# Kernel tuning notes

Measured on AMD Instinct MI355X. Metric: run time of the kernel, lower is better.

## Reference

```python
import jax, jax.numpy as jnp
import numpy as np

BIG_NEG = -1e9


def setup_inputs() -> dict:
    key = jax.random.key(0)
    ks = jax.random.split(key, 6)
    b, N1, d, C1, K = 4, 511, 64, 31, 32
    features = jax.random.normal(ks[0], (b, N1, d), jnp.float32)
    transition_logits = jax.random.normal(ks[1], (C1, C1), jnp.float32)
    init_logits = jax.random.uniform(ks[2], (C1,), jnp.float32)
    poisson_log_rates = jax.random.normal(ks[3], (C1,), jnp.float32) * 0.5 + 1.5
    A = jax.random.normal(ks[5], (d, d), jnp.float32)
    gaussian_cov = jnp.eye(d, dtype=jnp.float32) + 0.1 * (A @ A.T) / d
    gaussian_means = jax.random.normal(ks[4], (C1, d), jnp.float32) * 0.1
    return {
        "features": features,
        "transition_logits": transition_logits,
        "init_logits": init_logits,
        "poisson_log_rates": poisson_log_rates,
        "gaussian_means": gaussian_means,
        "gaussian_cov": gaussian_cov,
        "max_k": K,
        "add_eos": 1,
    }


def reference(features, transition_logits, init_logits, poisson_log_rates,
              gaussian_means, gaussian_cov, max_k, add_eos):
    b, N1, d = features.shape
    C1 = transition_logits.shape[0]
    K = int(max_k)
    dt = features.dtype

    # transition log-probs: mask diagonal with BIG_NEG, normalize over axis 0 (torch dim=0)
    trans = jax.nn.log_softmax(
        jnp.where(jnp.eye(C1, dtype=bool), jnp.asarray(BIG_NEG, dt), transition_logits), axis=0)
    init = jax.nn.log_softmax(init_logits)

    # Poisson duration log-probs: k*log(rate) - rate - lgamma(k+1), k = 0..K-1
    rates = jnp.exp(poisson_log_rates)  # [C1]
    tsteps = jnp.arange(K, dtype=dt)[:, None]  # [K,1]
    length = tsteps * poisson_log_rates[None, :] - rates[None, :] - jax.scipy.special.gammaln(tsteps + 1.0)  # [K,C1]

    # Gaussian emission log-probs, shared full covariance across classes
    L = jnp.linalg.cholesky(gaussian_cov)
    Linv = jax.scipy.linalg.solve_triangular(L, jnp.eye(d, dtype=dt), lower=True)
    diff = features[:, :, None, :] - gaussian_means[None, None]          # [b,N1,C1,d]
    y = jnp.einsum('bncd,ed->bnce', diff, Linv)
    maha = jnp.sum(y * y, axis=-1)                                       # [b,N1,C1]
    logdet = 2.0 * jnp.sum(jnp.log(jnp.diag(L)))
    emis = -0.5 * (d * jnp.log(jnp.asarray(2.0 * jnp.pi, dt)) + logdet + maha)

    if add_eos:
        N, C = N1 + 1, C1 + 1
        trans_a = jnp.full((C, C), BIG_NEG, dt).at[:C1, :C1].set(trans).at[C1, :].set(0.0)
        init_a = jnp.full((C,), BIG_NEG, dt).at[:C1].set(init)
        length_a = jnp.full((K, C), BIG_NEG, dt).at[:, :C1].set(length).at[1, C1].set(0.0)
        emis_a = jnp.full((b, N, C), BIG_NEG, dt).at[:, :N1, :C1].set(emis).at[:, N1, C1].set(0.0)
    else:
        N, C = N1, C1
        trans_a, init_a, length_a, emis_a = trans, init, length, emis

    ep = jnp.pad(emis_a, ((0, 0), (0, K), (0, 0)))
    cs = jnp.concatenate([jnp.zeros((b, 1, C), dt), jnp.cumsum(ep, axis=1)], axis=1)  # [b,N+K+1,C]
    tt = jnp.arange(N - 1)[:, None]
    kk = jnp.arange(K)[None, :]
    win = cs[:, tt + kk] - cs[:, tt]  # [b, N-1, K, C]

    # edge scores: b x (N-1) x K x C_prev x C
    scores = (trans_a[None, None, None] +
              length_a[None, None, :, None, :] +
              win[:, :, :, None, :])
    scores = scores.at[:, 0].add(init_a[None, None, None, :])
    keos = jnp.arange(1, K)
    scores = scores.at[:, N - 1 - keos, keos].add(emis_a[:, N - 1][:, None, :, None])
    return scores
```

## Files before the change

### kernel.cpp

```cpp
#include <hip/hip_runtime.h>
#include <math.h>

#define BIG_NEG -1.0e9f

typedef float f4 __attribute__((ext_vector_type(4)));

constexpr int B  = 4;
constexpr int N1 = 511;
constexpr int C1 = 31;
constexpr int K  = 32;
constexpr int N  = N1 + 1;
constexpr int C  = C1 + 1;

constexpr int WS_TRANS = 0;
constexpr int WS_INIT  = 1024;
constexpr int WS_LEN   = 1056;
constexpr int WS_P     = 2080;
constexpr int WS_W     = 6176;
constexpr int WS_BIAS  = 8224;
constexpr int WS_EMIS  = 8256;

__global__ __launch_bounds__(512) void k_prep(const float* __restrict__ tl,
                                              const float* __restrict__ il,
                                              const float* __restrict__ plr,
                                              const float* __restrict__ cov,
                                              const float* __restrict__ means,
                                              float* __restrict__ ws) {
    __shared__ float M[64][132];
    __shared__ float fc[2][64];
    __shared__ float piv[64];
    __shared__ float rpiv_s[64];
    __shared__ float mu[C1][64];
    __shared__ float s_logdet;

    const int tid = threadIdx.x;
    const int ii = tid >> 3;
    const int cg = tid & 7;

    f4* Mrow = (f4*)&M[ii][0];

    for (int idx = tid; idx < 1024; idx += 512) {
        const int i = idx >> 5, j = idx & 31;
        float lv;
        if (j < C1) {
            float lr = plr[j];
            lv = (float)i * lr - expf(lr) - lgammaf((float)i + 1.0f);
        } else {
            lv = (i == 1) ? 0.0f : BIG_NEG;
        }
        ws[WS_LEN + idx] = lv;
        if (i == C1) ws[WS_TRANS + idx] = 0.0f;
        else if (j == C1) ws[WS_TRANS + idx] = BIG_NEG;
    }
    if (tid < B * C) {
        const int bb = tid >> 5, cc = tid & 31;
        ws[WS_EMIS + (bb * N + N1) * C + cc] = (cc == C1) ? 0.0f : BIG_NEG;
    }
    if (tid < C1) {
        const int jj = tid;
        float m = BIG_NEG;
        for (int r = 0; r < C1; ++r) {
            float v = (r == jj) ? BIG_NEG : tl[r * C1 + jj];
            m = fmaxf(m, v);
        }
        float s = 0.0f;
        for (int r = 0; r < C1; ++r) {
            float v = (r == jj) ? BIG_NEG : tl[r * C1 + jj];
            s += expf(v - m);
        }
        float lse = m + logf(s);
        for (int r = 0; r < C1; ++r) {
            float v = (r == jj) ? BIG_NEG : tl[r * C1 + jj];
            ws[WS_TRANS + r * 32 + jj] = v - lse;
        }
    }
    if (tid == 32) {
        float m = -1.0e30f;
        for (int cc = 0; cc < C1; ++cc) m = fmaxf(m, il[cc]);
        float s = 0.0f;
        for (int cc = 0; cc < C1; ++cc) s += expf(il[cc] - m);
        float lse = m + logf(s);
        for (int cc = 0; cc < C1; ++cc) ws[WS_INIT + cc] = il[cc] - lse;
        ws[WS_INIT + C1] = BIG_NEG;
    }

    {
        Mrow[cg]     = *(const f4*)&cov[ii * 64 + 4 * cg];
        Mrow[cg + 8] = *(const f4*)&cov[ii * 64 + 4 * (cg + 8)];
        const int r0 = 4 * cg, r1 = 4 * (cg + 8);
        f4 e1 = {(ii == r0) ? 1.f : 0.f, (ii == r0 + 1) ? 1.f : 0.f,
                 (ii == r0 + 2) ? 1.f : 0.f, (ii == r0 + 3) ? 1.f : 0.f};
        f4 e2 = {(ii == r1) ? 1.f : 0.f, (ii == r1 + 1) ? 1.f : 0.f,
                 (ii == r1 + 2) ? 1.f : 0.f, (ii == r1 + 3) ? 1.f : 0.f};
        Mrow[cg + 16] = e1;
        Mrow[cg + 24] = e2;
    }
    if (cg == 0) fc[0][ii] = cov[ii * 64];
    for (int idx = tid; idx < C1 * 64; idx += 512)
        mu[idx >> 6][idx & 63] = means[idx];
    __syncthreads();

    for (int jj = 0; jj < 64; ++jj) {
        const int par = jj & 1;
        const float p = fc[par][jj];
        const float f = fc[par][ii] / p;
        if (tid == 0) piv[jj] = p;
        const f4* Mjj = (const f4*)&M[jj][0];
        const bool upd = (ii != jj);
#pragma unroll
        for (int h = 0; h < 4; ++h) {
            const int q = cg + 8 * h;
            const int k0 = 4 * q;
            const bool active = (k0 < 64) ? (k0 + 3 >= jj) : (k0 - 64 <= jj);
            if (!active) continue;
            f4 v = Mrow[q];
            if (upd) {
                v = v - f * Mjj[q];
                Mrow[q] = v;
            }
            if (jj < 63 && (unsigned)(jj + 1 - k0) < 4u) {
                const int d = jj + 1 - k0;
                fc[par ^ 1][ii] = (d == 0) ? v.x : (d == 1) ? v.y
                                 : (d == 2) ? v.z : v.w;
            }
        }
        __syncthreads();
    }

    if (tid < 64) {
        float lp = logf(piv[tid]);
        rpiv_s[tid] = 1.0f / piv[tid];
        for (int m2 = 32; m2 >= 1; m2 >>= 1) lp += __shfl_xor(lp, m2, 64);
        if (tid == 0) s_logdet = lp;
    }
    __syncthreads();

    {
        const float rp = rpiv_s[ii];
        f4 a = Mrow[16 + cg] * rp;
        f4 b = Mrow[24 + cg] * rp;
        *(f4*)&ws[WS_P + ii * 64 + 4 * cg] = a;
        *(f4*)&ws[WS_P + ii * 64 + 32 + 4 * cg] = b;
    }

    {
        const int c = tid >> 4;
        const int l = tid & 15;
        if (c < C1) {
            const f4* muc = (const f4*)&mu[c][0];
            float qacc = 0.0f;
#pragma unroll
            for (int h = 0; h < 4; ++h) {
                const int dd = l + 16 * h;
                const f4* Mr = (const f4*)&M[dd][64];
                f4 a4 = {0.f, 0.f, 0.f, 0.f};
#pragma unroll
                for (int e4 = 0; e4 < 16; ++e4) a4 += Mr[e4] * muc[e4];
                float a = (a4.x + a4.y) + (a4.z + a4.w);
                a *= rpiv_s[dd];
                ws[WS_W + dd * 32 + c] = a;
                qacc += a * mu[c][dd];
            }
            for (int m2 = 8; m2 >= 1; m2 >>= 1) qacc += __shfl_xor(qacc, m2, 64);
            if (l == 0)
                ws[WS_BIAS + c] =
                    -0.5f * (64.0f * 1.8378770664093453f + s_logdet + qacc);
        }
    }
}

__global__ __launch_bounds__(256) void k_emis(const float* __restrict__ feat,
                                              float* __restrict__ ws) {
    const int tid = threadIdx.x;
    const int w = tid >> 6, lane = tid & 63;
    const int flat = blockIdx.x * 4 + w;
    const int b = flat / N1, n = flat % N1;
    __shared__ float xs[4][64];

    const float x = feat[flat * 64 + lane];
    xs[w][lane] = x;

    const float* __restrict__ P = ws + WS_P;
    float z = 0.0f;
    for (int dd = 0; dd < 64; ++dd) z += P[dd * 64 + lane] * xs[w][dd];

    float xz = x * z;
    for (int m = 32; m >= 1; m >>= 1) xz += __shfl_xor(xz, m);

    float val = BIG_NEG;
    if (lane < C1) {
        float s = ws[WS_BIAS + lane] - 0.5f * xz;
        const float* __restrict__ wT = ws + WS_W;
        for (int dd = 0; dd < 64; ++dd) s += wT[dd * 32 + lane] * xs[w][dd];
        val = s;
    }
    if (lane < C) ws[WS_EMIS + (b * N + n) * C + lane] = val;
}

__global__ __launch_bounds__(256) void k_main(const float* __restrict__ ws,
                                              float* __restrict__ out) {
    const int bid = blockIdx.x;
    const int b = bid / N1, t = bid % N1;
    const int tid = threadIdx.x;
    __shared__ float sh[32][36];

    {
        const int row = tid >> 3;
        const int c4 = (tid & 7) << 2;
        f4 v = {0.f, 0.f, 0.f, 0.f};
        if (t + row < N)
            v = *(const f4*)&ws[WS_EMIS + (b * N + t + row) * C + c4];
        *(f4*)&sh[row][c4] = v;
    }
    __syncthreads();

    {
        const int sc = tid >> 3;
        const int g  = tid & 7;
        float p0 = sh[4 * g + 0][sc];
        float p1 = p0 + sh[4 * g + 1][sc];
        float p2 = p1 + sh[4 * g + 2][sc];
        float p3 = p2 + sh[4 * g + 3][sc];
        float sum = p3;
#pragma unroll
        for (int off = 1; off < 8; off <<= 1) {
            float nv = __shfl_up(sum, off, 8);
            if (g >= off) sum += nv;
        }
        const float excl = sum - p3;
        sh[4 * g + 0][sc] = p0 + excl;
        sh[4 * g + 1][sc] = p1 + excl;
        sh[4 * g + 2][sc] = p2 + excl;
        sh[4 * g + 3][sc] = p3 + excl;
    }

    const int cp = tid >> 3;
    const int c0 = (tid & 7) << 2;
    f4 pre = *(const f4*)&ws[WS_TRANS + cp * 32 + c0];
    if (t == 0) {
        f4 in4 = *(const f4*)&ws[WS_INIT + c0];
        pre = pre + in4;
    }
    const float emisN = (cp == C1) ? 0.0f : BIG_NEG;
    const int keos = N1 - t;
    const size_t obase = (size_t)bid * (K * C * C) + (size_t)(cp * 32 + c0);
    __syncthreads();

#pragma unroll 4
    for (int k = 0; k < K; ++k) {
        f4 len4 = *(const f4*)&ws[WS_LEN + k * 32 + c0];
        f4 w4 = {0.f, 0.f, 0.f, 0.f};
        if (k > 0) w4 = *(const f4*)&sh[k - 1][c0];
        f4 o = pre + len4 + w4;
        if (k == keos) o = o + emisN;
        *(f4*)&out[obase + (size_t)k * (C * C)] = o;
    }
}

extern "C" void kernel_launch(void* const* d_in, const int* in_sizes, int n_in,
                              void* d_out, int out_size, void* d_ws, size_t ws_size,
                              hipStream_t stream) {
    const float* feat = (const float*)d_in[0];
    const float* tl   = (const float*)d_in[1];
    const float* il   = (const float*)d_in[2];
    const float* plr  = (const float*)d_in[3];
    const float* gm   = (const float*)d_in[4];
    const float* gc   = (const float*)d_in[5];
    float* ws  = (float*)d_ws;
    float* out = (float*)d_out;

    hipLaunchKernelGGL(k_prep, dim3(1), dim3(512), 0, stream, tl, il, plr, gc, gm, ws);
    hipLaunchKernelGGL(k_emis, dim3(B * N1 / 4), dim3(256), 0, stream, feat, ws);
    hipLaunchKernelGGL(k_main, dim3(B * N1), dim3(256), 0, stream, ws, out);
}
```

Baseline: 98.66 us.

## Fuse emission computation into main kernel and block Cholesky elimination by two

Removes the separate emission kernel. Each main-kernel block now recomputes the emission log-probs for its 32-row window directly from the features, using P and a transposed W layout in the workspace. This saves a launch and the global round trip, at the cost of recomputing each emission row up to 32 times. The single-block Gauss-Jordan elimination in the prep kernel now processes two pivots per step with reciprocal intrinsics, halving the number of block barriers on that serial critical path.

Result: slower. 246.3 us (+149.6%).

```diff
diff --git a/kernel.cpp b/kernel.cpp
--- a/kernel.cpp
+++ b/kernel.cpp
@@ -16,9 +16,8 @@
 constexpr int WS_INIT  = 1024;
 constexpr int WS_LEN   = 1056;
 constexpr int WS_P     = 2080;
-constexpr int WS_W     = 6176;
+constexpr int WS_W2    = 6176;
 constexpr int WS_BIAS  = 8224;
-constexpr int WS_EMIS  = 8256;
 
 __global__ __launch_bounds__(512) void k_prep(const float* __restrict__ tl,
                                               const float* __restrict__ il,
@@ -27,7 +26,8 @@
                                               const float* __restrict__ means,
                                               float* __restrict__ ws) {
     __shared__ float M[64][132];
-    __shared__ float fc[2][64];
+    __shared__ float cA[2][64];
+    __shared__ float cB[2][64];
     __shared__ float piv[64];
     __shared__ float rpiv_s[64];
     __shared__ float mu[C1][64];
@@ -51,10 +51,6 @@
         ws[WS_LEN + idx] = lv;
         if (i == C1) ws[WS_TRANS + idx] = 0.0f;
         else if (j == C1) ws[WS_TRANS + idx] = BIG_NEG;
-    }
-    if (tid < B * C) {
-        const int bb = tid >> 5, cc = tid & 31;
-        ws[WS_EMIS + (bb * N + N1) * C + cc] = (cc == C1) ? 0.0f : BIG_NEG;
     }
     if (tid < C1) {
         const int jj = tid;
@@ -95,33 +91,53 @@
         Mrow[cg + 16] = e1;
         Mrow[cg + 24] = e2;
     }
-    if (cg == 0) fc[0][ii] = cov[ii * 64];
+    if (cg == 0) {
+        cA[0][ii] = cov[ii * 64];
+        cB[0][ii] = cov[ii * 64 + 1];
+    }
     for (int idx = tid; idx < C1 * 64; idx += 512)
         mu[idx >> 6][idx & 63] = means[idx];
     __syncthreads();
 
-    for (int jj = 0; jj < 64; ++jj) {
-        const int par = jj & 1;
-        const float p = fc[par][jj];
-        const float f = fc[par][ii] / p;
-        if (tid == 0) piv[jj] = p;
-        const f4* Mjj = (const f4*)&M[jj][0];
-        const bool upd = (ii != jj);
+    for (int s = 0; s < 64; s += 2) {
+        const int par = (s >> 1) & 1;
+        const float a1   = cA[par][ii];
+        const float b1   = cB[par][ii];
+        const float p1   = cA[par][s];
+        const float cb_s = cB[par][s];
+        const float a1p  = cA[par][s + 1];
+        const float b1p  = cB[par][s + 1];
+        const float rp1 = __builtin_amdgcn_rcpf(p1);
+        const float f1_i = a1 * rp1;
+        const float f1_p = a1p * rp1;
+        const float p2 = b1p - f1_p * cb_s;
+        const float rp2 = __builtin_amdgcn_rcpf(p2);
+        float aa, g1, g2;
+        if (ii == s) {
+            const float f2 = cb_s * rp2;
+            aa = 1.0f + f2 * f1_p; g1 = 0.0f; g2 = f2;
+        } else if (ii == s + 1) {
+            aa = 1.0f; g1 = f1_p; g2 = 0.0f;
+        } else {
+            const float f2 = (b1 - f1_i * cb_s) * rp2;
+            aa = 1.0f; g1 = f1_i - f2 * f1_p; g2 = f2;
+        }
+        if (tid == 0) { piv[s] = p1; piv[s + 1] = p2; }
+        const f4* Ms  = (const f4*)&M[s][0];
+        const f4* Ms1 = (const f4*)&M[s + 1][0];
+        const int pubk0 = (s + 2) & ~3;
 #pragma unroll
         for (int h = 0; h < 4; ++h) {
             const int q = cg + 8 * h;
             const int k0 = 4 * q;
-            const bool active = (k0 < 64) ? (k0 + 3 >= jj) : (k0 - 64 <= jj);
+            const bool active = (k0 < 64) ? (k0 + 3 >= s) : (k0 - 64 <= s + 1);
             if (!active) continue;
-            f4 v = Mrow[q];
-            if (upd) {
-                v = v - f * Mjj[q];
-                Mrow[q] = v;
-            }
-            if (jj < 63 && (unsigned)(jj + 1 - k0) < 4u) {
-                const int d = jj + 1 - k0;
-                fc[par ^ 1][ii] = (d == 0) ? v.x : (d == 1) ? v.y
-                                 : (d == 2) ? v.z : v.w;
+            f4 v = aa * Mrow[q] - g1 * Ms[q] - g2 * Ms1[q];
+            Mrow[q] = v;
+            if (s < 62 && k0 == pubk0) {
+                const int d = (s + 2) & 3;
+                cA[par ^ 1][ii] = (d == 0) ? v.x : v.z;
+                cB[par ^ 1][ii] = (d == 0) ? v.y : v.w;
             }
         }
         __syncthreads();
@@ -158,7 +174,7 @@
                 for (int e4 = 0; e4 < 16; ++e4) a4 += Mr[e4] * muc[e4];
                 float a = (a4.x + a4.y) + (a4.z + a4.w);
                 a *= rpiv_s[dd];
-                ws[WS_W + dd * 32 + c] = a;
+                ws[WS_W2 + c * 64 + dd] = a;
                 qacc += a * mu[c][dd];
             }
             for (int m2 = 8; m2 >= 1; m2 >>= 1) qacc += __shfl_xor(qacc, m2, 64);
@@ -169,48 +185,54 @@
     }
 }
 
-__global__ __launch_bounds__(256) void k_emis(const float* __restrict__ feat,
-                                              float* __restrict__ ws) {
-    const int tid = threadIdx.x;
-    const int w = tid >> 6, lane = tid & 63;
-    const int flat = blockIdx.x * 4 + w;
-    const int b = flat / N1, n = flat % N1;
-    __shared__ float xs[4][64];
-
-    const float x = feat[flat * 64 + lane];
-    xs[w][lane] = x;
-
-    const float* __restrict__ P = ws + WS_P;
-    float z = 0.0f;
-    for (int dd = 0; dd < 64; ++dd) z += P[dd * 64 + lane] * xs[w][dd];
-
-    float xz = x * z;
-    for (int m = 32; m >= 1; m >>= 1) xz += __shfl_xor(xz, m);
-
-    float val = BIG_NEG;
-    if (lane < C1) {
-        float s = ws[WS_BIAS + lane] - 0.5f * xz;
-        const float* __restrict__ wT = ws + WS_W;
-        for (int dd = 0; dd < 64; ++dd) s += wT[dd * 32 + lane] * xs[w][dd];
-        val = s;
-    }
-    if (lane < C) ws[WS_EMIS + (b * N + n) * C + lane] = val;
-}
-
-__global__ __launch_bounds__(256) void k_main(const float* __restrict__ ws,
+__global__ __launch_bounds__(256) void k_main(const float* __restrict__ feat,
+                                              const float* __restrict__ ws,
                                               float* __restrict__ out) {
     const int bid = blockIdx.x;
     const int b = bid / N1, t = bid % N1;
     const int tid = threadIdx.x;
+    const int w = tid >> 6, lane = tid & 63;
+    __shared__ float sx[32][64];
     __shared__ float sh[32][36];
 
-    {
-        const int row = tid >> 3;
-        const int c4 = (tid & 7) << 2;
+#pragma unroll
+    for (int rep = 0; rep < 2; ++rep) {
+        const int fi = tid + 256 * rep;
+        const int row = fi >> 4;
+        const int c4 = (fi & 15) << 2;
+        const int n = t + row;
         f4 v = {0.f, 0.f, 0.f, 0.f};
-        if (t + row < N)
-            v = *(const f4*)&ws[WS_EMIS + (b * N + t + row) * C + c4];
-        *(f4*)&sh[row][c4] = v;
+        if (n < N1) v = *(const f4*)&feat[(b * N1 + n) * 64 + c4];
+        *(f4*)&sx[row][c4] = v;
+    }
+    __syncthreads();
+
+    for (int r = w; r < 32; r += 4) {
+        const int n = t + r;
+        float val;
+        if (n < N1) {
+            const f4* xr = (const f4*)&sx[r][0];
+            const f4* Pr = (const f4*)&ws[WS_P + lane * 64];
+            f4 acc4 = {0.f, 0.f, 0.f, 0.f};
+#pragma unroll
+            for (int e = 0; e < 16; ++e) acc4 += Pr[e] * xr[e];
+            float xz = sx[r][lane] * ((acc4.x + acc4.y) + (acc4.z + acc4.w));
+            for (int m2 = 32; m2 >= 1; m2 >>= 1) xz += __shfl_xor(xz, m2);
+            val = BIG_NEG;
+            if (lane < C1) {
+                const f4* Wr = (const f4*)&ws[WS_W2 + lane * 64];
+                f4 wa = {0.f, 0.f, 0.f, 0.f};
+#pragma unroll
+                for (int e = 0; e < 16; ++e) wa += Wr[e] * xr[e];
+                val = ws[WS_BIAS + lane] - 0.5f * xz +
+                      ((wa.x + wa.y) + (wa.z + wa.w));
+            }
+        } else if (n == N1) {
+            val = (lane == C1) ? 0.0f : BIG_NEG;
+        } else {
+            val = 0.0f;
+        }
+        if (lane < 32) sh[r][lane] = val;
     }
     __syncthreads();
 
@@ -270,6 +292,5 @@
     float* out = (float*)d_out;
 
     hipLaunchKernelGGL(k_prep, dim3(1), dim3(512), 0, stream, tl, il, plr, gc, gm, ws);
-    hipLaunchKernelGGL(k_emis, dim3(B * N1 / 4), dim3(256), 0, stream, feat, ws);
-    hipLaunchKernelGGL(k_main, dim3(B * N1), dim3(256), 0, stream, ws, out);
+    hipLaunchKernelGGL(k_main, dim3(B * N1), dim3(256), 0, stream, feat, ws, out);
 }
```

## Block the covariance elimination into 4x4 pivot panels to cut barrier count

Applied to the files above, without the earlier changes.

Rewrites the Gauss-Jordan elimination in the prep kernel so that it processes four pivot columns per step, solving a 4x4 LU per panel. This cuts the sequential loop from 64 to 16 iterations and removes three quarters of the block barriers. The final scaling uses the saved 4x4 blocks to recover the inverse factor, and the log-determinant is taken as the log of a running product. The cost is more arithmetic per step and a risk of float overflow or underflow in that determinant product.

Result: faster. 79.98 us (-18.9%).

```diff
diff --git a/kernel.cpp b/kernel.cpp
--- a/kernel.cpp
+++ b/kernel.cpp
@@ -27,11 +27,9 @@
                                               const float* __restrict__ means,
                                               float* __restrict__ ws) {
     __shared__ float M[64][132];
-    __shared__ float fc[2][64];
-    __shared__ float piv[64];
-    __shared__ float rpiv_s[64];
+    __shared__ float cP[2][4][64];
+    __shared__ float Bsave[16][16];
     __shared__ float mu[C1][64];
-    __shared__ float s_logdet;
 
     const int tid = threadIdx.x;
     const int ii = tid >> 3;
@@ -95,53 +93,132 @@
         Mrow[cg + 16] = e1;
         Mrow[cg + 24] = e2;
     }
-    if (cg == 0) fc[0][ii] = cov[ii * 64];
+    if (cg == 0) {
+        cP[0][0][ii] = cov[ii * 64 + 0];
+        cP[0][1][ii] = cov[ii * 64 + 1];
+        cP[0][2][ii] = cov[ii * 64 + 2];
+        cP[0][3][ii] = cov[ii * 64 + 3];
+    }
     for (int idx = tid; idx < C1 * 64; idx += 512)
         mu[idx >> 6][idx & 63] = means[idx];
     __syncthreads();
 
-    for (int jj = 0; jj < 64; ++jj) {
-        const int par = jj & 1;
-        const float p = fc[par][jj];
-        const float f = fc[par][ii] / p;
-        if (tid == 0) piv[jj] = p;
-        const f4* Mjj = (const f4*)&M[jj][0];
-        const bool upd = (ii != jj);
+    float detprod = 1.0f;
+    for (int st = 0; st < 16; ++st) {
+        const int s = st << 2;
+        const int par = st & 1;
+        const float T00 = cP[par][0][s + 0], T01 = cP[par][0][s + 1],
+                    T02 = cP[par][0][s + 2], T03 = cP[par][0][s + 3];
+        const float T10 = cP[par][1][s + 0], T11 = cP[par][1][s + 1],
+                    T12 = cP[par][1][s + 2], T13 = cP[par][1][s + 3];
+        const float T20 = cP[par][2][s + 0], T21 = cP[par][2][s + 1],
+                    T22 = cP[par][2][s + 2], T23 = cP[par][2][s + 3];
+        const float T30 = cP[par][3][s + 0], T31 = cP[par][3][s + 1],
+                    T32 = cP[par][3][s + 2], T33 = cP[par][3][s + 3];
+        const float r0 = __builtin_amdgcn_rcpf(T00);
+        const float l10 = T10 * r0, l20 = T20 * r0, l30 = T30 * r0;
+        const float u11 = T11 - l10 * T01, u12 = T12 - l10 * T02,
+                    u13 = T13 - l10 * T03;
+        const float r1 = __builtin_amdgcn_rcpf(u11);
+        const float l21 = (T21 - l20 * T01) * r1;
+        const float l31 = (T31 - l30 * T01) * r1;
+        const float u22 = T22 - l20 * T02 - l21 * u12;
+        const float u23 = T23 - l20 * T03 - l21 * u13;
+        const float u32 = T32 - l30 * T02 - l31 * u12;
+        const float u33t = T33 - l30 * T03 - l31 * u13;
+        const float r2 = __builtin_amdgcn_rcpf(u22);
+        const float l32 = u32 * r2;
+        const float u33 = u33t - l32 * u23;
+        const float r3 = __builtin_amdgcn_rcpf(u33);
+        detprod *= T00 * u11 * u22 * u33;
+
+        if (tid < 16) Bsave[st][tid] = cP[par][tid & 3][s + (tid >> 2)];
+
+        const float m0 = cP[par][0][ii], m1 = cP[par][1][ii],
+                    m2 = cP[par][2][ii], m3 = cP[par][3][ii];
+        const float y0 = m0;
+        const float y1 = m1 - l10 * y0;
+        const float y2 = m2 - l20 * y0 - l21 * y1;
+        const float y3 = m3 - l30 * y0 - l31 * y1 - l32 * y2;
+        float g3 = y3 * r3;
+        float g2 = (y2 - u23 * g3) * r2;
+        float g1 = (y1 - u12 * g2 - u13 * g3) * r1;
+        float g0 = (y0 - T01 * g1 - T02 * g2 - T03 * g3) * r0;
+        const bool pivrow = (unsigned)(ii - s) < 4u;
+        if (pivrow) { g0 = 0.f; g1 = 0.f; g2 = 0.f; g3 = 0.f; }
+
+        const f4* Ms0 = (const f4*)&M[s + 0][0];
+        const f4* Ms1 = (const f4*)&M[s + 1][0];
+        const f4* Ms2 = (const f4*)&M[s + 2][0];
+        const f4* Ms3 = (const f4*)&M[s + 3][0];
+        const int qpub = st + 1;
 #pragma unroll
         for (int h = 0; h < 4; ++h) {
             const int q = cg + 8 * h;
             const int k0 = 4 * q;
-            const bool active = (k0 < 64) ? (k0 + 3 >= jj) : (k0 - 64 <= jj);
+            const bool active = (k0 < 64) ? (k0 + 3 >= s) : (k0 - 64 <= s + 3);
             if (!active) continue;
-            f4 v = Mrow[q];
-            if (upd) {
-                v = v - f * Mjj[q];
-                Mrow[q] = v;
+            f4 v = Mrow[q] - g0 * Ms0[q] - g1 * Ms1[q]
+                           - g2 * Ms2[q] - g3 * Ms3[q];
+            if (!pivrow) Mrow[q] = v;
+            if (st < 15 && q == qpub) {
+                cP[par ^ 1][0][ii] = v.x;
+                cP[par ^ 1][1][ii] = v.y;
+                cP[par ^ 1][2][ii] = v.z;
+                cP[par ^ 1][3][ii] = v.w;
             }
-            if (jj < 63 && (unsigned)(jj + 1 - k0) < 4u) {
-                const int d = jj + 1 - k0;
-                fc[par ^ 1][ii] = (d == 0) ? v.x : (d == 1) ? v.y
-                                 : (d == 2) ? v.z : v.w;
-            }
         }
         __syncthreads();
     }
 
-    if (tid < 64) {
-        float lp = logf(piv[tid]);
-        rpiv_s[tid] = 1.0f / piv[tid];
-        for (int m2 = 32; m2 >= 1; m2 >>= 1) lp += __shfl_xor(lp, m2, 64);
-        if (tid == 0) s_logdet = lp;
+    {
+        const int kb = ii >> 2, rsel = ii & 3, base = kb << 2;
+        const float* Bk = &Bsave[kb][0];
+        const float T00 = Bk[0],  T01 = Bk[4],  T02 = Bk[8],  T03 = Bk[12];
+        const float T10 = Bk[1],  T11 = Bk[5],  T12 = Bk[9],  T13 = Bk[13];
+        const float T20 = Bk[2],  T21 = Bk[6],  T22 = Bk[10], T23 = Bk[14];
+        const float T30 = Bk[3],  T31 = Bk[7],  T32 = Bk[11], T33 = Bk[15];
+        const float r0 = __builtin_amdgcn_rcpf(T00);
+        const float l10 = T10 * r0, l20 = T20 * r0, l30 = T30 * r0;
+        const float u11 = T11 - l10 * T01, u12 = T12 - l10 * T02,
+                    u13 = T13 - l10 * T03;
+        const float r1 = __builtin_amdgcn_rcpf(u11);
+        const float l21 = (T21 - l20 * T01) * r1;
+        const float l31 = (T31 - l30 * T01) * r1;
+        const float u22 = T22 - l20 * T02 - l21 * u12;
+        const float u23 = T23 - l20 * T03 - l21 * u13;
+        const float u32 = T32 - l30 * T02 - l31 * u12;
+        const float u33t = T33 - l30 * T03 - l31 * u13;
+        const float r2 = __builtin_amdgcn_rcpf(u22);
+        const float l32 = u32 * r2;
+        const float u33 = u33t - l32 * u23;
+        const float r3 = __builtin_amdgcn_rcpf(u33);
+        const float m0 = (rsel == 0) ? 1.f : 0.f;
+        const float m1 = (rsel == 1) ? 1.f : 0.f;
+        const float m2 = (rsel == 2) ? 1.f : 0.f;
+        const float m3 = (rsel == 3) ? 1.f : 0.f;
+        const float y0 = m0;
+        const float y1 = m1 - l10 * y0;
+        const float y2 = m2 - l20 * y0 - l21 * y1;
+        const float y3 = m3 - l30 * y0 - l31 * y1 - l32 * y2;
+        const float x3 = y3 * r3;
+        const float x2 = (y2 - u23 * x3) * r2;
+        const float x1 = (y1 - u12 * x2 - u13 * x3) * r1;
+        const float x0 = (y0 - T01 * x1 - T02 * x2 - T03 * x3) * r0;
+
+        const f4* R0 = (const f4*)&M[base + 0][64];
+        const f4* R1 = (const f4*)&M[base + 1][64];
+        const f4* R2 = (const f4*)&M[base + 2][64];
+        const f4* R3 = (const f4*)&M[base + 3][64];
+        f4 va = x0 * R0[cg] + x1 * R1[cg] + x2 * R2[cg] + x3 * R3[cg];
+        f4 vb = x0 * R0[cg + 8] + x1 * R1[cg + 8] +
+                x2 * R2[cg + 8] + x3 * R3[cg + 8];
+        *(f4*)&ws[WS_P + ii * 64 + 4 * cg] = va;
+        *(f4*)&ws[WS_P + ii * 64 + 32 + 4 * cg] = vb;
+        *(f4*)&M[ii][4 * cg] = va;
+        *(f4*)&M[ii][32 + 4 * cg] = vb;
     }
     __syncthreads();
-
-    {
-        const float rp = rpiv_s[ii];
-        f4 a = Mrow[16 + cg] * rp;
-        f4 b = Mrow[24 + cg] * rp;
-        *(f4*)&ws[WS_P + ii * 64 + 4 * cg] = a;
-        *(f4*)&ws[WS_P + ii * 64 + 32 + 4 * cg] = b;
-    }
 
     {
         const int c = tid >> 4;
@@ -152,19 +229,18 @@
 #pragma unroll
             for (int h = 0; h < 4; ++h) {
                 const int dd = l + 16 * h;
-                const f4* Mr = (const f4*)&M[dd][64];
+                const f4* Mr = (const f4*)&M[dd][0];
                 f4 a4 = {0.f, 0.f, 0.f, 0.f};
 #pragma unroll
                 for (int e4 = 0; e4 < 16; ++e4) a4 += Mr[e4] * muc[e4];
                 float a = (a4.x + a4.y) + (a4.z + a4.w);
-                a *= rpiv_s[dd];
                 ws[WS_W + dd * 32 + c] = a;
                 qacc += a * mu[c][dd];
             }
             for (int m2 = 8; m2 >= 1; m2 >>= 1) qacc += __shfl_xor(qacc, m2, 64);
             if (l == 0)
-                ws[WS_BIAS + c] =
-                    -0.5f * (64.0f * 1.8378770664093453f + s_logdet + qacc);
+                ws[WS_BIAS + c] = -0.5f * (64.0f * 1.8378770664093453f +
+                                           logf(detprod) + qacc);
         }
     }
 }
```
